# Optimization experiments

Measured on AMD Instinct MI355X. Metric: run time of the kernel, lower is better.

Reference implementation:

```python
import jax, jax.numpy as jnp
import numpy as np

N_HEADS = 32
N_KV_HEADS = 8
HEAD_DIM = 128
N_REP = N_HEADS // N_KV_HEADS


def apply_rope(x, cos, sin):
    # x: [B, S, H, D]; cos/sin: [S_max, D//2]
    S = x.shape[1]
    c = cos[:S][None, :, None, :]
    s = sin[:S][None, :, None, :]
    x_even = x[..., ::2]
    x_odd = x[..., 1::2]
    out = jnp.stack([x_even * c - x_odd * s, x_even * s + x_odd * c], axis=-1)
    return out.reshape(x.shape)


def setup_inputs() -> dict:
    key = jax.random.key(0)
    ks = jax.random.split(key, 8)
    B, S, D = 2, 2048, 4096
    x = jax.random.normal(ks[0], (B, S, D), dtype=jnp.float32)
    # RoPE tables
    pos = jnp.arange(S, dtype=jnp.float32)[:, None]
    inv_freq = 1.0 / (10000.0 ** (jnp.arange(0, HEAD_DIM, 2, dtype=jnp.float32) / HEAD_DIM))
    ang = pos * inv_freq[None, :]  # [S, HEAD_DIM//2]
    cos = jnp.cos(ang)
    sin = jnp.sin(ang)
    # causal additive mask [1,1,S,S]
    tril = jnp.tril(jnp.ones((S, S), dtype=bool))
    mask = jnp.where(tril, 0.0, -1e9).astype(jnp.float32)[None, None]
    sc = 0.02
    Wq = jax.random.normal(ks[1], (D, N_HEADS * HEAD_DIM), dtype=jnp.float32) * sc
    Wk = jax.random.normal(ks[2], (D, N_KV_HEADS * HEAD_DIM), dtype=jnp.float32) * sc
    Wv = jax.random.normal(ks[3], (D, N_KV_HEADS * HEAD_DIM), dtype=jnp.float32) * sc
    Wo = jax.random.normal(ks[4], (N_HEADS * HEAD_DIM, D), dtype=jnp.float32) * sc
    return {"x": x, "cos": cos, "sin": sin, "mask": mask,
            "Wq": Wq, "Wk": Wk, "Wv": Wv, "Wo": Wo}


def reference(x, cos, sin, mask, Wq, Wk, Wv, Wo):
    B, S, D = x.shape
    q = (x @ Wq).reshape(B, S, N_HEADS, HEAD_DIM)
    k = (x @ Wk).reshape(B, S, N_KV_HEADS, HEAD_DIM)
    v = (x @ Wv).reshape(B, S, N_KV_HEADS, HEAD_DIM)
    q = apply_rope(q, cos, sin)
    k = apply_rope(k, cos, sin)
    # repeat_interleave KV heads to match query heads
    k = jnp.repeat(k, N_REP, axis=2)
    v = jnp.repeat(v, N_REP, axis=2)
    q = q.transpose(0, 2, 1, 3)  # [B, H, S, D]
    k = k.transpose(0, 2, 1, 3)
    v = v.transpose(0, 2, 1, 3)
    scale = HEAD_DIM ** -0.5
    scores = jnp.einsum('bhqd,bhkd->bhqk', q, k) * scale + mask
    attn = jax.nn.softmax(scores, axis=-1)
    out = jnp.einsum('bhqk,bhkd->bhqd', attn, v)
    out = out.transpose(0, 2, 1, 3).reshape(B, S, N_HEADS * HEAD_DIM)
    return out @ Wo
```

## Files before the change

### kernel.cpp

```cpp
#include <hip/hip_runtime.h>

typedef __attribute__((ext_vector_type(8))) short short8;
typedef __attribute__((ext_vector_type(4))) float f32x4;
typedef __attribute__((ext_vector_type(4))) unsigned short u16x4;
typedef __attribute__((ext_vector_type(8))) unsigned short u16x8;

typedef __attribute__((address_space(3))) void lds_void;
typedef __attribute__((address_space(1))) void g_void;

#define GL16(g, l) __builtin_amdgcn_global_load_lds((g_void*)(g), (lds_void*)(l), 16, 0, 0)
#define EXP2F(x) __builtin_exp2f(x)

__device__ inline float b2f(unsigned short u) {
  union { unsigned u; float f; } v; v.u = ((unsigned)u) << 16; return v.f;
}
__device__ inline unsigned short f2b(float f) {
  union { float f; unsigned u; } v; v.f = f;
  unsigned r = v.u + 0x7FFFu + ((v.u >> 16) & 1u);
  return (unsigned short)(r >> 16);
}
__device__ inline unsigned short f2b_rne(float f) {
  unsigned u;
  asm("v_cvt_pk_bf16_f32 %0, %1, %2" : "=v"(u) : "v"(f), "v"(f));
  return (unsigned short)u;
}
__device__ inline unsigned short cvtb(float v) { return f2b(v); }
__device__ inline unsigned short cvtb(unsigned short v) { return v; }

__global__ __launch_bounds__(256) void conv_f32_bf16(const float* __restrict__ in,
                                                     unsigned short* __restrict__ out, long n) {
  long i = ((long)blockIdx.x * 256 + threadIdx.x) * 4;
  if (i >= n) return;
  f32x4 v = *(const f32x4*)(in + i);
  u16x4 o;
  o[0] = f2b(v[0]); o[1] = f2b(v[1]); o[2] = f2b(v[2]); o[3] = f2b(v[3]);
  *(u16x4*)(out + i) = o;
}

template <typename TIN>
__global__ __launch_bounds__(256) void transpose_bf16(const TIN* __restrict__ in,
                                                      unsigned short* __restrict__ out,
                                                      int R, int C, int ldin) {
  __shared__ unsigned short tile[32][33];
  int c0 = blockIdx.x * 32, r0 = blockIdx.y * 32;
  int tx = threadIdx.x & 31, ty = threadIdx.x >> 5;
#pragma unroll
  for (int i = ty; i < 32; i += 8)
    tile[i][tx] = cvtb(in[(long)(r0 + i) * ldin + c0 + tx]);
  __syncthreads();
#pragma unroll
  for (int i = ty; i < 32; i += 8)
    out[(long)(c0 + i) * R + r0 + tx] = tile[tx][i];
}

__global__ __launch_bounds__(256) void rope_kernel(unsigned short* __restrict__ QK,
                                                   const float* __restrict__ cosp,
                                                   const float* __restrict__ sinp,
                                                   int ld, int hshift, int smask,
                                                   float scale, int total) {
  int idx = blockIdx.x * 256 + threadIdx.x;
  if (idx >= total) return;
  int seg = idx & 15;
  int hh = (idx >> 4) & ((1 << hshift) - 1);
  int row = idx >> (4 + hshift);
  int s = row & smask;
  int d0 = seg << 3;
  unsigned short* p = QK + (long)row * ld + hh * 128 + d0;
  u16x8 v = *(const u16x8*)p;
  u16x8 o;
  int ib = d0 >> 1;
#pragma unroll
  for (int q = 0; q < 4; q++) {
    float c = cosp[s * 64 + ib + q];
    float sn = sinp[s * 64 + ib + q];
    float e = b2f(v[2 * q]), od = b2f(v[2 * q + 1]);
    o[2 * q]     = f2b((e * c - od * sn) * scale);
    o[2 * q + 1] = f2b((e * sn + od * c) * scale);
  }
  *(u16x8*)p = o;
}

template <bool OUT_BF16>
__global__ __launch_bounds__(256) void gemm_bt(const unsigned short* __restrict__ A,
                                               const unsigned short* __restrict__ Bt,
                                               void* __restrict__ C, int M, int N, int K) {
  __shared__ unsigned short As[128 * 32];
  __shared__ unsigned short Bs[128 * 32];
  const int tid = threadIdx.x;
  const int wave = tid >> 6, lane = tid & 63;
  const int lrow = lane & 15, kgrp = lane >> 4;
  const int nb = N >> 7;
  const int bm = blockIdx.x / nb, bn = blockIdx.x % nb;
  const int wr = wave >> 1, wc = wave & 1;

  f32x4 acc[4][4];
#pragma unroll
  for (int m = 0; m < 4; m++)
#pragma unroll
    for (int n = 0; n < 4; n++) acc[m][n] = (f32x4){0.f, 0.f, 0.f, 0.f};

  const char* ga = (const char*)(A + (long)(bm * 128 + (tid >> 2)) * K) + (tid & 3) * 16;
  const char* gb = (const char*)(Bt + (long)(bn * 128 + (tid >> 2)) * K) + (tid & 3) * 16;
  const long rowstep = (long)64 * K * 2;
  char* lA = (char*)As + wave * 1024;
  char* lB = (char*)Bs + wave * 1024;

  for (int k0 = 0; k0 < K; k0 += 32) {
    __syncthreads();
    GL16(ga + (long)k0 * 2, lA);
    GL16(ga + (long)k0 * 2 + rowstep, lA + 4096);
    GL16(gb + (long)k0 * 2, lB);
    GL16(gb + (long)k0 * 2 + rowstep, lB + 4096);
    __syncthreads();
    short8 af[4], bfv[4];
#pragma unroll
    for (int m = 0; m < 4; m++)
      af[m] = *(const short8*)(As + (wr * 64 + m * 16 + lrow) * 32 + kgrp * 8);
#pragma unroll
    for (int n = 0; n < 4; n++)
      bfv[n] = *(const short8*)(Bs + (wc * 64 + n * 16 + lrow) * 32 + kgrp * 8);
#pragma unroll
    for (int m = 0; m < 4; m++)
#pragma unroll
      for (int n = 0; n < 4; n++)
        acc[m][n] = __builtin_amdgcn_mfma_f32_16x16x32_bf16(af[m], bfv[n], acc[m][n], 0, 0, 0);
  }

  const long crow0 = (long)bm * 128 + wr * 64 + kgrp * 4;
  const int ccol0 = bn * 128 + wc * 64 + lrow;
#pragma unroll
  for (int m = 0; m < 4; m++)
#pragma unroll
    for (int n = 0; n < 4; n++)
#pragma unroll
      for (int r = 0; r < 4; r++) {
        long row = crow0 + m * 16 + r;
        int col = ccol0 + n * 16;
        if (OUT_BF16)
          ((unsigned short*)C)[row * N + col] = f2b(acc[m][n][r]);
        else
          ((float*)C)[row * N + col] = acc[m][n][r];
      }
}

__global__ __launch_bounds__(256) void attn_kernel(const unsigned short* __restrict__ QKV,
                                                   const unsigned short* __restrict__ Vt,
                                                   unsigned short* __restrict__ O,
                                                   int S, int BS) {
  __shared__ unsigned short Ks[64 * 128];
  __shared__ unsigned short Vs[128 * 64];
  __shared__ unsigned short Ps[4][16 * 68];
  const int tid = threadIdx.x, wave = tid >> 6, lane = tid & 63;
  const int lrow = lane & 15, kgrp = lane >> 4;
  const int nqt = S >> 6, nqt2 = nqt >> 1;
  int bid = blockIdx.x;
  const int qp = bid % nqt2; bid /= nqt2;
  const int h = bid & 31;
  const int b = bid >> 5;
  const int kh = h >> 2;
  const long rowbase = (long)b * S;

  const char* kg = (const char*)(QKV + rowbase * 6144 + 4096 + kh * 128)
                   + (tid >> 4) * 12288 + (((tid & 15) ^ ((tid >> 4) & 7)) * 16);
  const char* vg = (const char*)(Vt + (long)(kh * 128 + (tid >> 3)) * BS + rowbase)
                   + (((tid & 7) ^ ((tid >> 3) & 7)) * 16);
  char* lK = (char*)Ks + wave * 1024;
  char* lV = (char*)Vs + wave * 1024;

  for (int pass = 0; pass < 2; pass++) {
    const int qt = pass ? (nqt - 1 - qp) : qp;
    const int qbase = qt * 64;
    const int q0 = qbase + wave * 16;

    short8 qf[4];
    {
      const unsigned short* qpt = QKV + (rowbase + q0 + lrow) * 6144 + h * 128 + kgrp * 8;
#pragma unroll
      for (int dc = 0; dc < 4; dc++) qf[dc] = *(const short8*)(qpt + dc * 32);
    }
    f32x4 oacc[8];
#pragma unroll
    for (int dt = 0; dt < 8; dt++) oacc[dt] = (f32x4){0.f, 0.f, 0.f, 0.f};
    float mrun[4] = {-1e30f, -1e30f, -1e30f, -1e30f};
    float lrun[4] = {0.f, 0.f, 0.f, 0.f};

    const int kv_end = qbase + 64;
    for (int kv0 = 0; kv0 < kv_end; kv0 += 64) {
      __syncthreads();
#pragma unroll
      for (int p = 0; p < 4; p++)
        GL16(kg + (long)(kv0 + p * 16) * 12288, lK + p * 4096);
#pragma unroll
      for (int p = 0; p < 4; p++)
        GL16(vg + (long)kv0 * 2 + (long)p * 32 * BS * 2, lV + p * 4096);
      __syncthreads();

      f32x4 sc[4];
#pragma unroll
      for (int n = 0; n < 4; n++) {
        f32x4 s = (f32x4){0.f, 0.f, 0.f, 0.f};
#pragma unroll
        for (int dc = 0; dc < 4; dc++) {
          short8 kf = *(const short8*)(Ks + (n * 16 + lrow) * 128 + (((dc * 4 + kgrp) ^ (lrow & 7)) << 3));
          s = __builtin_amdgcn_mfma_f32_16x16x32_bf16(qf[dc], kf, s, 0, 0, 0);
        }
        sc[n] = s;
      }

      if (kv0 + 63 > q0) {
#pragma unroll
        for (int r = 0; r < 4; r++) {
          const int qg = q0 + kgrp * 4 + r;
#pragma unroll
          for (int n = 0; n < 4; n++) {
            int kgi = kv0 + n * 16 + lrow;
            if (kgi > qg) sc[n][r] = -1e30f;
          }
        }
      }

      float mx[4];
#pragma unroll
      for (int r = 0; r < 4; r++) {
        float m0 = fmaxf(fmaxf(sc[0][r], sc[1][r]), fmaxf(sc[2][r], sc[3][r]));
#pragma unroll
        for (int d = 1; d < 16; d <<= 1) m0 = fmaxf(m0, __shfl_xor(m0, d, 64));
        mx[r] = m0;
      }
      bool grow = false;
#pragma unroll
      for (int r = 0; r < 4; r++) grow = grow || (mx[r] > mrun[r] + 8.f);

      if (__all(!grow)) {
#pragma unroll
        for (int r = 0; r < 4; r++) {
          float psum = 0.f;
#pragma unroll
          for (int n = 0; n < 4; n++) {
            float pv = EXP2F(sc[n][r] - mrun[r]);
            psum += pv;
            Ps[wave][(kgrp * 4 + r) * 68 + n * 16 + lrow] = f2b_rne(pv);
          }
          lrun[r] += psum;
        }
      } else {
#pragma unroll
        for (int r = 0; r < 4; r++) {
          float mnew = fmaxf(mrun[r], mx[r]);
          float corr = EXP2F(mrun[r] - mnew);
          mrun[r] = mnew;
          float psum = 0.f;
#pragma unroll
          for (int n = 0; n < 4; n++) {
            float pv = EXP2F(sc[n][r] - mnew);
            psum += pv;
            Ps[wave][(kgrp * 4 + r) * 68 + n * 16 + lrow] = f2b_rne(pv);
          }
          lrun[r] = lrun[r] * corr + psum;
#pragma unroll
          for (int dt = 0; dt < 8; dt++) oacc[dt][r] *= corr;
        }
      }
      asm volatile("s_waitcnt lgkmcnt(0)" ::: "memory");
#pragma unroll
      for (int kc = 0; kc < 2; kc++) {
        short8 pa = *(const short8*)(&Ps[wave][lrow * 68 + kc * 32 + kgrp * 8]);
#pragma unroll
        for (int dt = 0; dt < 8; dt++) {
          short8 vb = *(const short8*)(Vs + (dt * 16 + lrow) * 64 + (((kc * 4 + kgrp) ^ (lrow & 7)) << 3));
          oacc[dt] = __builtin_amdgcn_mfma_f32_16x16x32_bf16(pa, vb, oacc[dt], 0, 0, 0);
        }
      }
    }

    float inv[4];
#pragma unroll
    for (int r = 0; r < 4; r++) {
      float l = lrun[r];
#pragma unroll
      for (int d = 1; d < 16; d <<= 1) l += __shfl_xor(l, d, 64);
      inv[r] = 1.f / l;
    }
    unsigned short* op = O + (rowbase + q0 + kgrp * 4) * 4096 + h * 128 + lrow;
#pragma unroll
    for (int dt = 0; dt < 8; dt++)
#pragma unroll
      for (int r = 0; r < 4; r++)
        op[(long)r * 4096 + dt * 16] = f2b_rne(oacc[dt][r] * inv[r]);
  }
}

extern "C" void kernel_launch(void* const* d_in, const int* in_sizes, int n_in,
                              void* d_out, int out_size, void* d_ws, size_t ws_size,
                              hipStream_t stream) {
  const float* x = (const float*)d_in[0];
  const float* cosp = (const float*)d_in[1];
  const float* sinp = (const float*)d_in[2];
  const float* Wq = (const float*)d_in[4];
  const float* Wk = (const float*)d_in[5];
  const float* Wv = (const float*)d_in[6];
  const float* Wo = (const float*)d_in[7];
  const int S = 2048;
  const long M = 4096;

  if (ws_size < 176160768ULL) return;

  char* ws = (char*)d_ws;
  unsigned short* xb   = (unsigned short*)(ws);
  unsigned short* Wqt  = (unsigned short*)(ws + 33554432);
  unsigned short* Wkt  = (unsigned short*)(ws + 67108864);
  unsigned short* Wvt  = (unsigned short*)(ws + 75497472);
  unsigned short* Wot  = (unsigned short*)(ws + 83886080);
  unsigned short* QKVb = (unsigned short*)(ws + 117440512);
  unsigned short* Vtg  = (unsigned short*)(ws + 167772160);
  unsigned short* AO   = xb;

  conv_f32_bf16<<<16384, 256, 0, stream>>>(x, xb, M * 4096);
  transpose_bf16<float><<<dim3(128, 128), 256, 0, stream>>>(Wq, Wqt, 4096, 4096, 4096);
  transpose_bf16<float><<<dim3(32, 128), 256, 0, stream>>>(Wk, Wkt, 4096, 1024, 1024);
  transpose_bf16<float><<<dim3(32, 128), 256, 0, stream>>>(Wv, Wvt, 4096, 1024, 1024);
  transpose_bf16<float><<<dim3(128, 128), 256, 0, stream>>>(Wo, Wot, 4096, 4096, 4096);

  gemm_bt<true><<<1536, 256, 0, stream>>>(xb, Wqt, QKVb, 4096, 6144, 4096);
  transpose_bf16<unsigned short><<<dim3(32, 128), 256, 0, stream>>>(QKVb + 5120, Vtg, 4096, 1024, 6144);

  const float qscale = 0.08838834764831845f * 1.44269504088896341f;
  rope_kernel<<<8192, 256, 0, stream>>>(QKVb, cosp, sinp, 6144, 5, S - 1, qscale, 4096 * 32 * 16);
  rope_kernel<<<2048, 256, 0, stream>>>(QKVb + 4096, cosp, sinp, 6144, 3, S - 1, 1.0f, 4096 * 8 * 16);

  attn_kernel<<<1024, 256, 0, stream>>>(QKVb, Vtg, AO, S, 4096);

  gemm_bt<false><<<1024, 256, 0, stream>>>(AO, Wot, d_out, 4096, 4096, 4096);
}
```

Measured before the change: 702.6 us.

## Replace GEMM with 256x256-tile 8-wave double-buffered kernel with swizzled LDS

Replaces the 128x128, single-buffered, 4-wave bf16 GEMM with a 256x256-tile, 8-wave kernel. It uses K=64 stages, double-buffered LDS filled by global_load_lds, an XOR-swizzled LDS layout to avoid bank conflicts, and block-index swizzling for L2 locality. The prefetch of the next A and B tiles overlaps the MFMA phases, and s_setprio raises wave priority during MFMA. The cost is heavy register pressure (128 accumulator floats per thread) and 128KB of LDS per block, plus fewer blocks for the output GEMM (256 on a 256-CU part), so occupancy and tail effects matter.

```diff
diff --git a/kernel.cpp b/kernel.cpp
--- a/kernel.cpp
+++ b/kernel.cpp
@@ -10,6 +10,7 @@
 
 #define GL16(g, l) __builtin_amdgcn_global_load_lds((g_void*)(g), (lds_void*)(l), 16, 0, 0)
 #define EXP2F(x) __builtin_exp2f(x)
+#define BARRIER() do { asm volatile("" ::: "memory"); __builtin_amdgcn_s_barrier(); asm volatile("" ::: "memory"); } while (0)
 
 __device__ inline float b2f(unsigned short u) {
   union { unsigned u; float f; } v; v.u = ((unsigned)u) << 16; return v.f;
@@ -81,65 +82,126 @@
 }
 
 template <bool OUT_BF16>
-__global__ __launch_bounds__(256) void gemm_bt(const unsigned short* __restrict__ A,
-                                               const unsigned short* __restrict__ Bt,
-                                               void* __restrict__ C, int M, int N, int K) {
-  __shared__ unsigned short As[128 * 32];
-  __shared__ unsigned short Bs[128 * 32];
+__global__ __launch_bounds__(512, 2) void gemm_bt8(const unsigned short* __restrict__ A,
+                                                   const unsigned short* __restrict__ Bt,
+                                                   void* __restrict__ C, int M, int N, int K) {
+  __shared__ unsigned short As[2 * 16384];
+  __shared__ unsigned short Bs[2 * 16384];
   const int tid = threadIdx.x;
-  const int wave = tid >> 6, lane = tid & 63;
-  const int lrow = lane & 15, kgrp = lane >> 4;
-  const int nb = N >> 7;
-  const int bm = blockIdx.x / nb, bn = blockIdx.x % nb;
-  const int wr = wave >> 1, wc = wave & 1;
-
-  f32x4 acc[4][4];
-#pragma unroll
-  for (int m = 0; m < 4; m++)
-#pragma unroll
-    for (int n = 0; n < 4; n++) acc[m][n] = (f32x4){0.f, 0.f, 0.f, 0.f};
-
-  const char* ga = (const char*)(A + (long)(bm * 128 + (tid >> 2)) * K) + (tid & 3) * 16;
-  const char* gb = (const char*)(Bt + (long)(bn * 128 + (tid >> 2)) * K) + (tid & 3) * 16;
-  const long rowstep = (long)64 * K * 2;
-  char* lA = (char*)As + wave * 1024;
-  char* lB = (char*)Bs + wave * 1024;
-
-  for (int k0 = 0; k0 < K; k0 += 32) {
-    __syncthreads();
-    GL16(ga + (long)k0 * 2, lA);
-    GL16(ga + (long)k0 * 2 + rowstep, lA + 4096);
-    GL16(gb + (long)k0 * 2, lB);
-    GL16(gb + (long)k0 * 2 + rowstep, lB + 4096);
-    __syncthreads();
-    short8 af[4], bfv[4];
-#pragma unroll
-    for (int m = 0; m < 4; m++)
-      af[m] = *(const short8*)(As + (wr * 64 + m * 16 + lrow) * 32 + kgrp * 8);
-#pragma unroll
-    for (int n = 0; n < 4; n++)
-      bfv[n] = *(const short8*)(Bs + (wc * 64 + n * 16 + lrow) * 32 + kgrp * 8);
-#pragma unroll
-    for (int m = 0; m < 4; m++)
-#pragma unroll
-      for (int n = 0; n < 4; n++)
-        acc[m][n] = __builtin_amdgcn_mfma_f32_16x16x32_bf16(af[m], bfv[n], acc[m][n], 0, 0, 0);
+  const int wid = tid >> 6, lane = tid & 63;
+  const int lrow = lane & 15, kq = lane >> 4;
+  const int wr = wid >> 2, wc = wid & 3;
+  const int nbn = N >> 8;
+  const int nwg = (M >> 8) * nbn;
+  const int bid = blockIdx.x;
+  const int cpx = nwg >> 3;
+  const int swz = (bid & 7) * cpx + (bid >> 3);
+  const int bm = swz / nbn, bn = swz % nbn;
+
+  const long K2 = (long)K * 2;
+  const long csw = (long)(((tid & 7) ^ ((tid >> 3) & 7)) << 4);
+  const char* gA = (const char*)A + ((long)bm * 256 + (tid >> 3)) * K2 + csw;
+  const char* gB = (const char*)Bt + ((long)bn * 256 + (tid >> 3)) * K2 + csw;
+
+#define STAGE4(gbase, lbase) do { \
+    GL16((gbase),            (lbase)); \
+    GL16((gbase) + 64 * K2,  (char*)(lbase) + 8192); \
+    GL16((gbase) + 128 * K2, (char*)(lbase) + 16384); \
+    GL16((gbase) + 192 * K2, (char*)(lbase) + 24576); } while (0)
+
+  f32x4 acc[8][4];
+#pragma unroll
+  for (int mf = 0; mf < 8; mf++)
+#pragma unroll
+    for (int nf = 0; nf < 4; nf++) acc[mf][nf] = (f32x4){0.f, 0.f, 0.f, 0.f};
+
+  const int arow = (wr * 128 + lrow) * 64;
+  const int brow = (wc * 64 + lrow) * 64;
+  const int ax = lrow & 7;
+
+  STAGE4(gA, (char*)As + wid * 1024);
+  STAGE4(gB, (char*)Bs + wid * 1024);
+  STAGE4(gB + 128, (char*)Bs + 32768 + wid * 1024);
+  asm volatile("s_waitcnt vmcnt(0)" ::: "memory");
+  BARRIER();
+
+  const int NT = K >> 6;
+  for (int t = 0; t < NT; ++t) {
+    const int c = t & 1;
+    const unsigned short* Ab = As + c * 16384;
+    const unsigned short* Bb = Bs + c * 16384;
+    const long koff = (long)t << 7;
+
+    short8 bf[4][2], af[2][2];
+#pragma unroll
+    for (int nf = 0; nf < 4; nf++)
+#pragma unroll
+      for (int kk = 0; kk < 2; kk++)
+        bf[nf][kk] = *(const short8*)&Bb[brow + nf * 1024 + (((kk * 4 + kq) ^ ax) << 3)];
+#pragma unroll
+    for (int mf = 0; mf < 2; mf++)
+#pragma unroll
+      for (int kk = 0; kk < 2; kk++)
+        af[mf][kk] = *(const short8*)&Ab[arow + mf * 1024 + (((kk * 4 + kq) ^ ax) << 3)];
+    if (t + 1 < NT) STAGE4(gA + koff + 128, (char*)As + (c ^ 1) * 32768 + wid * 1024);
+    BARRIER();
+    __builtin_amdgcn_s_setprio(1);
+#pragma unroll
+    for (int mf = 0; mf < 2; mf++)
+#pragma unroll
+      for (int nf = 0; nf < 4; nf++)
+#pragma unroll
+        for (int kk = 0; kk < 2; kk++)
+          acc[mf][nf] = __builtin_amdgcn_mfma_f32_16x16x32_bf16(af[mf][kk], bf[nf][kk], acc[mf][nf], 0, 0, 0);
+    __builtin_amdgcn_s_setprio(0);
+    BARRIER();
+
+#pragma unroll
+    for (int ph = 1; ph < 4; ph++) {
+      const int mb = ph * 2;
+      short8 af2[2][2];
+#pragma unroll
+      for (int mf = 0; mf < 2; mf++)
+#pragma unroll
+        for (int kk = 0; kk < 2; kk++)
+          af2[mf][kk] = *(const short8*)&Ab[arow + (mb + mf) * 1024 + (((kk * 4 + kq) ^ ax) << 3)];
+      if (ph == 1 && t + 2 < NT) STAGE4(gB + koff + 256, (char*)Bs + c * 32768 + wid * 1024);
+      BARRIER();
+      __builtin_amdgcn_s_setprio(1);
+#pragma unroll
+      for (int mf = 0; mf < 2; mf++)
+#pragma unroll
+        for (int nf = 0; nf < 4; nf++)
+#pragma unroll
+          for (int kk = 0; kk < 2; kk++)
+            acc[mb + mf][nf] = __builtin_amdgcn_mfma_f32_16x16x32_bf16(af2[mf][kk], bf[nf][kk], acc[mb + mf][nf], 0, 0, 0);
+      __builtin_amdgcn_s_setprio(0);
+      BARRIER();
+    }
+
+    if (t + 2 < NT) {
+      asm volatile("s_waitcnt vmcnt(4)" ::: "memory");
+    } else if (t + 1 < NT) {
+      asm volatile("s_waitcnt vmcnt(0)" ::: "memory");
+    }
+    BARRIER();
   }
-
-  const long crow0 = (long)bm * 128 + wr * 64 + kgrp * 4;
-  const int ccol0 = bn * 128 + wc * 64 + lrow;
-#pragma unroll
-  for (int m = 0; m < 4; m++)
-#pragma unroll
-    for (int n = 0; n < 4; n++)
+#undef STAGE4
+
+  const long crow0 = (long)bm * 256 + wr * 128 + kq * 4;
+  const int ccol0 = bn * 256 + wc * 64 + lrow;
+#pragma unroll
+  for (int mf = 0; mf < 8; mf++)
+#pragma unroll
+    for (int nf = 0; nf < 4; nf++)
 #pragma unroll
       for (int r = 0; r < 4; r++) {
-        long row = crow0 + m * 16 + r;
-        int col = ccol0 + n * 16;
+        long row = crow0 + mf * 16 + r;
+        int col = ccol0 + nf * 16;
         if (OUT_BF16)
-          ((unsigned short*)C)[row * N + col] = f2b(acc[m][n][r]);
+          ((unsigned short*)C)[row * N + col] = f2b(acc[mf][nf][r]);
         else
-          ((float*)C)[row * N + col] = acc[m][n][r];
+          ((float*)C)[row * N + col] = acc[mf][nf][r];
       }
 }
 
@@ -321,7 +383,7 @@
   transpose_bf16<float><<<dim3(32, 128), 256, 0, stream>>>(Wv, Wvt, 4096, 1024, 1024);
   transpose_bf16<float><<<dim3(128, 128), 256, 0, stream>>>(Wo, Wot, 4096, 4096, 4096);
 
-  gemm_bt<true><<<1536, 256, 0, stream>>>(xb, Wqt, QKVb, 4096, 6144, 4096);
+  gemm_bt8<true><<<384, 512, 0, stream>>>(xb, Wqt, QKVb, 4096, 6144, 4096);
   transpose_bf16<unsigned short><<<dim3(32, 128), 256, 0, stream>>>(QKVb + 5120, Vtg, 4096, 1024, 6144);
 
   const float qscale = 0.08838834764831845f * 1.44269504088896341f;
@@ -330,5 +392,5 @@
 
   attn_kernel<<<1024, 256, 0, stream>>>(QKVb, Vtg, AO, S, 4096);
 
-  gemm_bt<false><<<1024, 256, 0, stream>>>(AO, Wot, d_out, 4096, 4096, 4096);
-}
+  gemm_bt8<false><<<256, 512, 0, stream>>>(AO, Wot, d_out, 4096, 4096, 4096);
+}
```

Result: faster. 631.7 us (-10.1%).

## Double-buffer GEMM with swizzled LDS, block remap, and fused RoPE epilogue

Applied to the files above, without the earlier changes.

Replaces the single-buffered GEMM with one that uses a 64-wide K step, two LDS buffers that prefetch the next tile while MFMAs run, an XOR-swizzled LDS layout to avoid bank conflicts, grouped block-index remapping for L2 reuse, and raised wave priority around the MFMAs. RoPE and the Q scaling move into the QKV GEMM epilogue through a lane shuffle, so the two separate RoPE kernels and their extra pass over QKV memory are gone. The cost is more LDS per block (64KB) and cos/sin loads inside the epilogue. The epilogue also changes rounding slightly, since RoPE is now applied to fp32 accumulators before the bf16 conversion.

```diff
diff --git a/kernel.cpp b/kernel.cpp
--- a/kernel.cpp
+++ b/kernel.cpp
@@ -10,6 +10,7 @@
 
 #define GL16(g, l) __builtin_amdgcn_global_load_lds((g_void*)(g), (lds_void*)(l), 16, 0, 0)
 #define EXP2F(x) __builtin_exp2f(x)
+#define BARRIER() do { asm volatile("" ::: "memory"); __builtin_amdgcn_s_barrier(); asm volatile("" ::: "memory"); } while (0)
 
 __device__ inline float b2f(unsigned short u) {
   union { unsigned u; float f; } v; v.u = ((unsigned)u) << 16; return v.f;
@@ -53,81 +54,92 @@
     out[(long)(c0 + i) * R + r0 + tx] = tile[tx][i];
 }
 
-__global__ __launch_bounds__(256) void rope_kernel(unsigned short* __restrict__ QK,
-                                                   const float* __restrict__ cosp,
-                                                   const float* __restrict__ sinp,
-                                                   int ld, int hshift, int smask,
-                                                   float scale, int total) {
-  int idx = blockIdx.x * 256 + threadIdx.x;
-  if (idx >= total) return;
-  int seg = idx & 15;
-  int hh = (idx >> 4) & ((1 << hshift) - 1);
-  int row = idx >> (4 + hshift);
-  int s = row & smask;
-  int d0 = seg << 3;
-  unsigned short* p = QK + (long)row * ld + hh * 128 + d0;
-  u16x8 v = *(const u16x8*)p;
-  u16x8 o;
-  int ib = d0 >> 1;
-#pragma unroll
-  for (int q = 0; q < 4; q++) {
-    float c = cosp[s * 64 + ib + q];
-    float sn = sinp[s * 64 + ib + q];
-    float e = b2f(v[2 * q]), od = b2f(v[2 * q + 1]);
-    o[2 * q]     = f2b((e * c - od * sn) * scale);
-    o[2 * q + 1] = f2b((e * sn + od * c) * scale);
+template <int MODE>
+__global__ __launch_bounds__(256, 2) void gemm128(const unsigned short* __restrict__ A,
+                                                  const unsigned short* __restrict__ Bt,
+                                                  void* __restrict__ C,
+                                                  const float* __restrict__ cosp,
+                                                  const float* __restrict__ sinp,
+                                                  int M, int N, int K) {
+  __shared__ unsigned short As[2][128 * 64];
+  __shared__ unsigned short Bs[2][128 * 64];
+  const int tid = threadIdx.x;
+  const int wid = tid >> 6, lane = tid & 63;
+  const int lrow = lane & 15, kq = lane >> 4;
+  const int wr = wid >> 1, wc = wid & 1;
+  const int nbn = N >> 7;
+  const int nwg = (M >> 7) * nbn;
+  const int bid = blockIdx.x;
+  const int swz = (bid & 7) * (nwg >> 3) + (bid >> 3);
+  const int bm = swz / nbn, bn = swz % nbn;
+
+  const long K2 = (long)K * 2;
+  const long csw = (long)(((tid & 7) ^ ((tid >> 3) & 7)) << 4);
+  const char* gA = (const char*)A + ((long)bm * 128 + (tid >> 3)) * K2 + csw;
+  const char* gB = (const char*)Bt + ((long)bn * 128 + (tid >> 3)) * K2 + csw;
+
+#define STAGEAB(buf, koff) do { \
+    char* _da = (char*)As + (buf) * 16384 + tid * 16; \
+    char* _db = (char*)Bs + (buf) * 16384 + tid * 16; \
+    GL16(gA + (koff),               _da); \
+    GL16(gA + (koff) + 32 * K2,     _da + 4096); \
+    GL16(gA + (koff) + 64 * K2,     _da + 8192); \
+    GL16(gA + (koff) + 96 * K2,     _da + 12288); \
+    GL16(gB + (koff),               _db); \
+    GL16(gB + (koff) + 32 * K2,     _db + 4096); \
+    GL16(gB + (koff) + 64 * K2,     _db + 8192); \
+    GL16(gB + (koff) + 96 * K2,     _db + 12288); } while (0)
+
+  f32x4 acc[4][4];
+#pragma unroll
+  for (int m = 0; m < 4; m++)
+#pragma unroll
+    for (int n = 0; n < 4; n++) acc[m][n] = (f32x4){0.f, 0.f, 0.f, 0.f};
+
+  const int arow = (wr * 64 + lrow) * 64;
+  const int brow = (wc * 64 + lrow) * 64;
+  const int ax = lrow & 7;
+
+  STAGEAB(0, 0);
+
+  const int NT = K >> 6;
+  for (int t = 0; t < NT; ++t) {
+    const int c = t & 1;
+    BARRIER();
+    if (t + 1 < NT) {
+      STAGEAB(c ^ 1, (long)(t + 1) << 7);
+      asm volatile("s_waitcnt vmcnt(8)" ::: "memory");
+    } else {
+      asm volatile("s_waitcnt vmcnt(0)" ::: "memory");
+    }
+    const unsigned short* Ab = As[0] + c * 8192;
+    const unsigned short* Bb = Bs[0] + c * 8192;
+    short8 af[4][2], bfv[4][2];
+#pragma unroll
+    for (int m = 0; m < 4; m++)
+#pragma unroll
+      for (int kk = 0; kk < 2; kk++)
+        af[m][kk] = *(const short8*)&Ab[arow + m * 1024 + (((kk * 4 + kq) ^ ax) << 3)];
+#pragma unroll
+    for (int n = 0; n < 4; n++)
+#pragma unroll
+      for (int kk = 0; kk < 2; kk++)
+        bfv[n][kk] = *(const short8*)&Bb[brow + n * 1024 + (((kk * 4 + kq) ^ ax) << 3)];
+    __builtin_amdgcn_s_setprio(1);
+#pragma unroll
+    for (int m = 0; m < 4; m++)
+#pragma unroll
+      for (int n = 0; n < 4; n++)
+#pragma unroll
+        for (int kk = 0; kk < 2; kk++)
+          acc[m][n] = __builtin_amdgcn_mfma_f32_16x16x32_bf16(af[m][kk], bfv[n][kk], acc[m][n], 0, 0, 0);
+    __builtin_amdgcn_s_setprio(0);
   }
-  *(u16x8*)p = o;
-}
-
-template <bool OUT_BF16>
-__global__ __launch_bounds__(256) void gemm_bt(const unsigned short* __restrict__ A,
-                                               const unsigned short* __restrict__ Bt,
-                                               void* __restrict__ C, int M, int N, int K) {
-  __shared__ unsigned short As[128 * 32];
-  __shared__ unsigned short Bs[128 * 32];
-  const int tid = threadIdx.x;
-  const int wave = tid >> 6, lane = tid & 63;
-  const int lrow = lane & 15, kgrp = lane >> 4;
-  const int nb = N >> 7;
-  const int bm = blockIdx.x / nb, bn = blockIdx.x % nb;
-  const int wr = wave >> 1, wc = wave & 1;
-
-  f32x4 acc[4][4];
-#pragma unroll
-  for (int m = 0; m < 4; m++)
-#pragma unroll
-    for (int n = 0; n < 4; n++) acc[m][n] = (f32x4){0.f, 0.f, 0.f, 0.f};
-
-  const char* ga = (const char*)(A + (long)(bm * 128 + (tid >> 2)) * K) + (tid & 3) * 16;
-  const char* gb = (const char*)(Bt + (long)(bn * 128 + (tid >> 2)) * K) + (tid & 3) * 16;
-  const long rowstep = (long)64 * K * 2;
-  char* lA = (char*)As + wave * 1024;
-  char* lB = (char*)Bs + wave * 1024;
-
-  for (int k0 = 0; k0 < K; k0 += 32) {
-    __syncthreads();
-    GL16(ga + (long)k0 * 2, lA);
-    GL16(ga + (long)k0 * 2 + rowstep, lA + 4096);
-    GL16(gb + (long)k0 * 2, lB);
-    GL16(gb + (long)k0 * 2 + rowstep, lB + 4096);
-    __syncthreads();
-    short8 af[4], bfv[4];
-#pragma unroll
-    for (int m = 0; m < 4; m++)
-      af[m] = *(const short8*)(As + (wr * 64 + m * 16 + lrow) * 32 + kgrp * 8);
-#pragma unroll
-    for (int n = 0; n < 4; n++)
-      bfv[n] = *(const short8*)(Bs + (wc * 64 + n * 16 + lrow) * 32 + kgrp * 8);
-#pragma unroll
-    for (int m = 0; m < 4; m++)
-#pragma unroll
-      for (int n = 0; n < 4; n++)
-        acc[m][n] = __builtin_amdgcn_mfma_f32_16x16x32_bf16(af[m], bfv[n], acc[m][n], 0, 0, 0);
-  }
-
-  const long crow0 = (long)bm * 128 + wr * 64 + kgrp * 4;
+#undef STAGEAB
+
+  const long crow0 = (long)bm * 128 + wr * 64 + kq * 4;
   const int ccol0 = bn * 128 + wc * 64 + lrow;
+  const float qscale = 0.08838834764831845f * 1.44269504088896341f;
 #pragma unroll
   for (int m = 0; m < 4; m++)
 #pragma unroll
@@ -136,10 +148,21 @@
       for (int r = 0; r < 4; r++) {
         long row = crow0 + m * 16 + r;
         int col = ccol0 + n * 16;
-        if (OUT_BF16)
-          ((unsigned short*)C)[row * N + col] = f2b(acc[m][n][r]);
-        else
-          ((float*)C)[row * N + col] = acc[m][n][r];
+        float v = acc[m][n][r];
+        if (MODE == 0) {
+          ((float*)C)[row * N + col] = v;
+        } else {
+          float other = __shfl_xor(v, 1, 64);
+          float out = v;
+          if (col < 5120) {
+            int s = (int)(row & 2047);
+            int ib = (col & 127) >> 1;
+            float cc = cosp[s * 64 + ib], ss = sinp[s * 64 + ib];
+            out = (col & 1) ? (other * ss + v * cc) : (v * cc - other * ss);
+            if (col < 4096) out *= qscale;
+          }
+          ((unsigned short*)C)[row * N + col] = f2b(out);
+        }
       }
 }
 
@@ -321,14 +344,10 @@
   transpose_bf16<float><<<dim3(32, 128), 256, 0, stream>>>(Wv, Wvt, 4096, 1024, 1024);
   transpose_bf16<float><<<dim3(128, 128), 256, 0, stream>>>(Wo, Wot, 4096, 4096, 4096);
 
-  gemm_bt<true><<<1536, 256, 0, stream>>>(xb, Wqt, QKVb, 4096, 6144, 4096);
+  gemm128<2><<<1536, 256, 0, stream>>>(xb, Wqt, QKVb, cosp, sinp, 4096, 6144, 4096);
   transpose_bf16<unsigned short><<<dim3(32, 128), 256, 0, stream>>>(QKVb + 5120, Vtg, 4096, 1024, 6144);
 
-  const float qscale = 0.08838834764831845f * 1.44269504088896341f;
-  rope_kernel<<<8192, 256, 0, stream>>>(QKVb, cosp, sinp, 6144, 5, S - 1, qscale, 4096 * 32 * 16);
-  rope_kernel<<<2048, 256, 0, stream>>>(QKVb + 4096, cosp, sinp, 6144, 3, S - 1, 1.0f, 4096 * 8 * 16);
-
   attn_kernel<<<1024, 256, 0, stream>>>(QKVb, Vtg, AO, S, 4096);
 
-  gemm_bt<false><<<1024, 256, 0, stream>>>(AO, Wot, d_out, 4096, 4096, 4096);
-}
+  gemm128<0><<<1024, 256, 0, stream>>>(AO, Wot, d_out, nullptr, nullptr, 4096, 4096, 4096);
+}
```

Result: faster. 686.4 us (-2.3%).
